# Kernel optimization log

Measured on AMD Instinct MI355X. Metric: run time of the kernel, lower is better.

The kernel has to match this reference:

```python
import jax, jax.numpy as jnp
import numpy as np

D = 2048      # hidden_size
H = 16        # num_attention_heads
KVH = 4       # num_key_value_heads
HD = 128      # head_dim
E = 32        # num_experts
TOPK = 8      # num_experts_per_tok
F = 768       # moe_intermediate_size
EPS = 1e-6
THETA = 1000000.0
B, S = 2, 1024


def setup_inputs() -> dict:
    key = jax.random.key(0)
    ks = jax.random.split(key, 16)
    sc = lambda *shape: 1.0 / np.sqrt(shape[-2] if len(shape) > 1 else shape[0])
    return {
        "hidden_states": jax.random.normal(ks[0], (B, S, D), jnp.float32),
        "attention_mask": jnp.ones((B, S), jnp.bool_),
        "input_ln_scale": jnp.ones((D,), jnp.float32),
        "post_ln_scale": jnp.ones((D,), jnp.float32),
        "q_w": jax.random.normal(ks[1], (D, H * HD), jnp.float32) * sc(D, H * HD),
        "k_w": jax.random.normal(ks[2], (D, KVH * HD), jnp.float32) * sc(D, KVH * HD),
        "v_w": jax.random.normal(ks[3], (D, KVH * HD), jnp.float32) * sc(D, KVH * HD),
        "o_w": jax.random.normal(ks[4], (H * HD, D), jnp.float32) * sc(H * HD, D),
        "q_norm_scale": jnp.ones((HD,), jnp.float32),
        "k_norm_scale": jnp.ones((HD,), jnp.float32),
        "gate_w": jax.random.normal(ks[5], (D, E), jnp.float32) * sc(D, E),
        "gate_proj": jax.random.normal(ks[6], (E, D, F), jnp.float32) * sc(E, D, F),
        "up_proj": jax.random.normal(ks[7], (E, D, F), jnp.float32) * sc(E, D, F),
        "down_proj": jax.random.normal(ks[8], (E, F, D), jnp.float32) * sc(E, F, D),
    }


def _rms(x, scale):
    return x * jax.lax.rsqrt(jnp.mean(x * x, axis=-1, keepdims=True) + EPS) * scale


def _rope(x):
    # x: [B, S, h, HD]
    half = HD // 2
    inv_freq = 1.0 / (THETA ** (jnp.arange(0, half, dtype=jnp.float32) / half))
    freqs = jnp.arange(x.shape[1], dtype=jnp.float32)[:, None] * inv_freq  # [S, HD/2]
    cos = jnp.concatenate([jnp.cos(freqs)] * 2, axis=-1)[None, :, None, :]
    sin = jnp.concatenate([jnp.sin(freqs)] * 2, axis=-1)[None, :, None, :]
    rot = jnp.concatenate([-x[..., half:], x[..., :half]], axis=-1)
    return x * cos + rot * sin


def _forward(hidden_states, attention_mask, input_ln_scale, post_ln_scale,
             q_w, k_w, v_w, o_w, q_norm_scale, k_norm_scale,
             gate_w, gate_proj, up_proj, down_proj):
    b, s, _ = hidden_states.shape
    residual = hidden_states
    h = _rms(hidden_states, input_ln_scale)

    # ---- Qwen3 attention (GQA + per-head RMSNorm + RoPE, causal) ----
    q = _rms((h @ q_w).reshape(b, s, H, HD), q_norm_scale)
    k = _rms((h @ k_w).reshape(b, s, KVH, HD), k_norm_scale)
    v = (h @ v_w).reshape(b, s, KVH, HD)
    q, k = _rope(q), _rope(k)
    rep = H // KVH
    k = jnp.repeat(k, rep, axis=2)  # [B,S,H,HD]
    v = jnp.repeat(v, rep, axis=2)
    scores = jnp.einsum('bqhd,bkhd->bhqk', q, k) * (HD ** -0.5)
    causal = jnp.tril(jnp.ones((s, s), jnp.bool_))
    mask = causal[None, None] & attention_mask[:, None, None, :]
    scores = jnp.where(mask, scores, jnp.finfo(scores.dtype).min)
    attn = jax.nn.softmax(scores, axis=-1)
    ctx = jnp.einsum('bhqk,bkhd->bqhd', attn, v).reshape(b, s, H * HD)
    h = residual + ctx @ o_w

    # ---- MoE block ----
    residual = h
    x = _rms(h, post_ln_scale).reshape(-1, D)  # [N, D]
    router_logits = x @ gate_w                 # [N, E]
    routing_weights, selected = jax.lax.top_k(router_logits, k=TOPK)
    routing_weights = jax.nn.softmax(routing_weights, axis=-1)
    sel_flat = jnp.ravel(selected)                     # [N*K]
    x_exp = jnp.repeat(x, TOPK, axis=0)                # [N*K, D]
    sort_idx = jnp.argsort(sel_flat)
    unsort_idx = jnp.argsort(sort_idx)
    x_sorted = x_exp[sort_idx]
    group_sizes = jnp.bincount(sel_flat, length=E)
    gate_out = jax.lax.ragged_dot(x_sorted, gate_proj, group_sizes)
    up_out = jax.lax.ragged_dot(x_sorted, up_proj, group_sizes)
    activated = jax.nn.silu(gate_out) * up_out
    down_out = jax.lax.ragged_dot(activated, down_proj, group_sizes)
    unsorted = down_out[unsort_idx].reshape(-1, TOPK, D)
    moe_out = (unsorted * routing_weights[..., None]).sum(axis=1).reshape(b, s, D)
    return residual + moe_out


def reference(hidden_states, attention_mask, input_ln_scale, post_ln_scale,
              q_w, k_w, v_w, o_w, q_norm_scale, k_norm_scale,
              gate_w, gate_proj, up_proj, down_proj):
    return _forward(hidden_states, attention_mask, input_ln_scale, post_ln_scale,
                    q_w, k_w, v_w, o_w, q_norm_scale, k_norm_scale,
                    gate_w, gate_proj, up_proj, down_proj)
```

## Files before the change

kernel.cpp:

```cpp
#include <hip/hip_runtime.h>
#include <hip/hip_bf16.h>

#define D_ 2048
#define H_ 16
#define KVH_ 4
#define HD_ 128
#define E_ 32
#define TOPK_ 8
#define F_ 768
#define NB_ 2
#define SS_ 1024
#define NT_ 2048
#define NPAIR_ 16384

typedef __attribute__((ext_vector_type(8))) short short8;
typedef __attribute__((ext_vector_type(4))) float floatx4;
typedef __attribute__((ext_vector_type(4))) unsigned int uintx4;
typedef __attribute__((ext_vector_type(4))) unsigned short ushortx4;

__device__ __forceinline__ unsigned short f2bf(float f) {
  union { float f; unsigned u; } v; v.f = f;
  unsigned r = v.u + 0x7FFFu + ((v.u >> 16) & 1u);
  return (unsigned short)(r >> 16);
}
__device__ __forceinline__ float bf2f(unsigned short h) {
  union { unsigned u; float f; } v; v.u = ((unsigned)h) << 16;
  return v.f;
}
__device__ __forceinline__ void split2(float v, unsigned short& hi, unsigned short& lo) {
  unsigned short h = f2bf(v);
  hi = h;
  lo = f2bf(v - bf2f(h));
}
__device__ __forceinline__ void gload16(const unsigned short* g, unsigned short* l) {
  __builtin_amdgcn_global_load_lds(
      (const __attribute__((address_space(1))) unsigned int*)g,
      (__attribute__((address_space(3))) unsigned int*)l, 16, 0, 0);
}

__global__ __launch_bounds__(256) void tconv_kernel(const float* __restrict__ src,
                                                    unsigned short* __restrict__ dst,
                                                    int R, int C) {
  size_t off = (size_t)blockIdx.z * R * C;
  src += off; dst += off;
  __shared__ float t[32][33];
  int c0 = blockIdx.x * 32, r0 = blockIdx.y * 32;
  int row = threadIdx.x >> 3, c4 = (threadIdx.x & 7) * 4;
  float4 v = *(const float4*)(src + (size_t)(r0 + row) * C + c0 + c4);
  t[row][c4 + 0] = v.x; t[row][c4 + 1] = v.y; t[row][c4 + 2] = v.z; t[row][c4 + 3] = v.w;
  __syncthreads();
  ushortx4 o = { f2bf(t[c4 + 0][row]), f2bf(t[c4 + 1][row]),
                 f2bf(t[c4 + 2][row]), f2bf(t[c4 + 3][row]) };
  *(ushortx4*)(dst + (size_t)(c0 + row) * R + r0 + c4) = o;
}

__global__ __launch_bounds__(256) void tsplit_kernel(const float* __restrict__ src,
                                                     unsigned short* __restrict__ dhi,
                                                     unsigned short* __restrict__ dlo,
                                                     int R, int C) {
  __shared__ float t[32][33];
  int c0 = blockIdx.x * 32, r0 = blockIdx.y * 32;
  int row = threadIdx.x >> 3, c4 = (threadIdx.x & 7) * 4;
  float4 v = *(const float4*)(src + (size_t)(r0 + row) * C + c0 + c4);
  t[row][c4 + 0] = v.x; t[row][c4 + 1] = v.y; t[row][c4 + 2] = v.z; t[row][c4 + 3] = v.w;
  __syncthreads();
  ushortx4 oh, ol;
  #pragma unroll
  for (int i = 0; i < 4; ++i) {
    unsigned short hi, lo;
    split2(t[c4 + i][row], hi, lo);
    oh[i] = hi; ol[i] = lo;
  }
  size_t didx = (size_t)(c0 + row) * R + r0 + c4;
  *(ushortx4*)(dhi + didx) = oh;
  *(ushortx4*)(dlo + didx) = ol;
}

template<int MODE>
__global__ __launch_bounds__(256) void rms_kernel(const float* __restrict__ in,
                                                  const float* __restrict__ sc,
                                                  float* __restrict__ outf,
                                                  unsigned short* __restrict__ o1,
                                                  unsigned short* __restrict__ o2) {
  __shared__ float red[4];
  int row = blockIdx.x, tid = threadIdx.x;
  const float4* x4 = (const float4*)(in + (size_t)row * D_);
  float4 a = x4[tid], b = x4[tid + 256];
  float ss = a.x*a.x + a.y*a.y + a.z*a.z + a.w*a.w
           + b.x*b.x + b.y*b.y + b.z*b.z + b.w*b.w;
  #pragma unroll
  for (int off = 1; off < 64; off <<= 1) ss += __shfl_xor(ss, off);
  if ((tid & 63) == 0) red[tid >> 6] = ss;
  __syncthreads();
  float r = rsqrtf((red[0] + red[1] + red[2] + red[3]) * (1.0f / D_) + 1e-6f);
  const float4* s4 = (const float4*)sc;
  float4 sa = s4[tid], sb = s4[tid + 256];
  float va[8] = { a.x*r*sa.x, a.y*r*sa.y, a.z*r*sa.z, a.w*r*sa.w,
                  b.x*r*sb.x, b.y*r*sb.y, b.z*r*sb.z, b.w*r*sb.w };
  if (MODE == 0) {
    ushortx4 h0, l0, h1, l1;
    #pragma unroll
    for (int i = 0; i < 4; ++i) { unsigned short h, l; split2(va[i], h, l); h0[i] = h; l0[i] = l; }
    #pragma unroll
    for (int i = 0; i < 4; ++i) { unsigned short h, l; split2(va[4 + i], h, l); h1[i] = h; l1[i] = l; }
    *(ushortx4*)(o1 + (size_t)row * D_ + tid * 4) = h0;
    *(ushortx4*)(o2 + (size_t)row * D_ + tid * 4) = l0;
    *(ushortx4*)(o1 + (size_t)row * D_ + 1024 + tid * 4) = h1;
    *(ushortx4*)(o2 + (size_t)row * D_ + 1024 + tid * 4) = l1;
  } else {
    *(float4*)(outf + (size_t)row * D_ + tid * 4) = make_float4(va[0], va[1], va[2], va[3]);
    *(float4*)(outf + (size_t)row * D_ + 1024 + tid * 4) = make_float4(va[4], va[5], va[6], va[7]);
    ushortx4 h0 = { f2bf(va[0]), f2bf(va[1]), f2bf(va[2]), f2bf(va[3]) };
    ushortx4 h1 = { f2bf(va[4]), f2bf(va[5]), f2bf(va[6]), f2bf(va[7]) };
    *(ushortx4*)(o1 + (size_t)row * D_ + tid * 4) = h0;
    *(ushortx4*)(o1 + (size_t)row * D_ + 1024 + tid * 4) = h1;
  }
}

template<int EPI>
__global__ __launch_bounds__(256) void gemm_bb(const unsigned short* __restrict__ Ahi,
                                               const unsigned short* __restrict__ Alo,
                                               const unsigned short* __restrict__ Bhi,
                                               const unsigned short* __restrict__ Blo,
                                               const float* __restrict__ res,
                                               float* __restrict__ out,
                                               int M, int Nn, int K) {
  __shared__ unsigned short Ah[64 * 72], Al[64 * 72], Bh[64 * 72], Bl[64 * 72];
  int tid = threadIdx.x, l = tid & 63, wid = tid >> 6;
  int lr = l & 15, lk = (l >> 4) * 8;
  int m0 = blockIdx.y * 64, n0 = blockIdx.x * 64;
  int wr = (wid >> 1) * 32, wc = (wid & 1) * 32;
  int srow = tid >> 3, sch = (tid & 7) * 8;
  size_t aoff[2], boff[2];
  int loff[2];
  #pragma unroll
  for (int i = 0; i < 2; ++i) {
    aoff[i] = (size_t)(m0 + i * 32 + srow) * K + sch;
    boff[i] = (size_t)(n0 + i * 32 + srow) * K + sch;
    loff[i] = (i * 32 + srow) * 72 + sch;
  }
  floatx4 acc[2][2];
  #pragma unroll
  for (int i = 0; i < 2; ++i)
    #pragma unroll
    for (int j = 0; j < 2; ++j) acc[i][j] = (floatx4){0.f, 0.f, 0.f, 0.f};
  for (int k0 = 0; k0 < K; k0 += 64) {
    uintx4 vah[2], val[2], vbh[2], vbl[2];
    #pragma unroll
    for (int i = 0; i < 2; ++i) {
      vah[i] = *(const uintx4*)(Ahi + aoff[i] + k0);
      val[i] = *(const uintx4*)(Alo + aoff[i] + k0);
      vbh[i] = *(const uintx4*)(Bhi + boff[i] + k0);
      vbl[i] = *(const uintx4*)(Blo + boff[i] + k0);
    }
    __syncthreads();
    #pragma unroll
    for (int i = 0; i < 2; ++i) {
      *(uintx4*)&Ah[loff[i]] = vah[i];
      *(uintx4*)&Al[loff[i]] = val[i];
      *(uintx4*)&Bh[loff[i]] = vbh[i];
      *(uintx4*)&Bl[loff[i]] = vbl[i];
    }
    __syncthreads();
    #pragma unroll
    for (int ks = 0; ks < 2; ++ks) {
      short8 ah[2], al_[2], bh[2], bl_[2];
      #pragma unroll
      for (int i = 0; i < 2; ++i) {
        ah[i]  = *(const short8*)&Ah[(wr + i * 16 + lr) * 72 + ks * 32 + lk];
        al_[i] = *(const short8*)&Al[(wr + i * 16 + lr) * 72 + ks * 32 + lk];
        bh[i]  = *(const short8*)&Bh[(wc + i * 16 + lr) * 72 + ks * 32 + lk];
        bl_[i] = *(const short8*)&Bl[(wc + i * 16 + lr) * 72 + ks * 32 + lk];
      }
      #pragma unroll
      for (int i = 0; i < 2; ++i)
        #pragma unroll
        for (int j = 0; j < 2; ++j) {
          acc[i][j] = __builtin_amdgcn_mfma_f32_16x16x32_bf16(ah[i], bh[j], acc[i][j], 0, 0, 0);
          acc[i][j] = __builtin_amdgcn_mfma_f32_16x16x32_bf16(ah[i], bl_[j], acc[i][j], 0, 0, 0);
          acc[i][j] = __builtin_amdgcn_mfma_f32_16x16x32_bf16(al_[i], bh[j], acc[i][j], 0, 0, 0);
        }
    }
  }
  int rq = (l >> 4) * 4;
  #pragma unroll
  for (int i = 0; i < 2; ++i)
    #pragma unroll
    for (int j = 0; j < 2; ++j)
      #pragma unroll
      for (int r = 0; r < 4; ++r) {
        size_t idx = (size_t)(m0 + wr + i * 16 + rq + r) * Nn + (n0 + wc + j * 16 + lr);
        float v = acc[i][j][r];
        if (EPI == 1) v += res[idx];
        out[idx] = v;
      }
}

template<int EPI>
__global__ __launch_bounds__(256) void gemm_bb128g(const unsigned short* __restrict__ Ahi,
                                                   const unsigned short* __restrict__ Alo,
                                                   const unsigned short* __restrict__ Bhi,
                                                   const unsigned short* __restrict__ Blo,
                                                   const float* __restrict__ res,
                                                   float* __restrict__ out,
                                                   int M, int Nn, int K) {
  int g = blockIdx.x;
  int nwg = gridDim.x;
  int per = nwg >> 3;
  int sw = (g & 7) * per + (g >> 3);
  int my = M >> 7;
  int xt = sw / my, yt = sw - xt * my;
  int m0 = yt * 128, n0 = xt * 128;
  __shared__ unsigned short Ah[2][128 * 32], Al[2][128 * 32];
  __shared__ unsigned short Bh[2][128 * 32], Bl[2][128 * 32];
  int tid = threadIdx.x, l = tid & 63, wid = tid >> 6;
  int lr = l & 15, lk = (l >> 4) * 8;
  int wr = (wid >> 1) * 64, wc = (wid & 1) * 64;
  int srl = l >> 2;
  int sch = ((l & 3) ^ (srl & 3)) * 8;
  size_t aoffs[2], boffs[2];
  int ldo[2];
  #pragma unroll
  for (int i = 0; i < 2; ++i) {
    int r = wid * 32 + i * 16 + srl;
    aoffs[i] = (size_t)(m0 + r) * K + sch;
    boffs[i] = (size_t)(n0 + r) * K + sch;
    ldo[i] = (wid * 32 + i * 16) * 32;
  }
  floatx4 acc[4][4];
  #pragma unroll
  for (int i = 0; i < 4; ++i)
    #pragma unroll
    for (int j = 0; j < 4; ++j) acc[i][j] = (floatx4){0.f, 0.f, 0.f, 0.f};

  auto stage = [&](int sel, int k0) {
    #pragma unroll
    for (int i = 0; i < 2; ++i) {
      gload16(Ahi + aoffs[i] + k0, &Ah[sel][ldo[i]]);
      gload16(Alo + aoffs[i] + k0, &Al[sel][ldo[i]]);
      gload16(Bhi + boffs[i] + k0, &Bh[sel][ldo[i]]);
      gload16(Blo + boffs[i] + k0, &Bl[sel][ldo[i]]);
    }
  };

  int rsw = ((l >> 4) ^ (lr & 3)) << 3;
  stage(0, 0);
  asm volatile("s_waitcnt vmcnt(0)" ::: "memory");
  __syncthreads();
  for (int k0 = 0; k0 < K; k0 += 32) {
    int cur = (k0 >> 5) & 1;
    if (k0 + 32 < K) stage(cur ^ 1, k0 + 32);
    short8 ah[4], al_[4];
    #pragma unroll
    for (int i = 0; i < 4; ++i) {
      int ao = (wr + i * 16 + lr) * 32 + rsw;
      ah[i]  = *(const short8*)&Ah[cur][ao];
      al_[i] = *(const short8*)&Al[cur][ao];
    }
    #pragma unroll
    for (int j = 0; j < 4; ++j) {
      int bo = (wc + j * 16 + lr) * 32 + rsw;
      short8 bh  = *(const short8*)&Bh[cur][bo];
      short8 bl_ = *(const short8*)&Bl[cur][bo];
      #pragma unroll
      for (int i = 0; i < 4; ++i) {
        acc[i][j] = __builtin_amdgcn_mfma_f32_16x16x32_bf16(ah[i], bh, acc[i][j], 0, 0, 0);
        acc[i][j] = __builtin_amdgcn_mfma_f32_16x16x32_bf16(ah[i], bl_, acc[i][j], 0, 0, 0);
        acc[i][j] = __builtin_amdgcn_mfma_f32_16x16x32_bf16(al_[i], bh, acc[i][j], 0, 0, 0);
      }
    }
    asm volatile("s_waitcnt vmcnt(0)" ::: "memory");
    __syncthreads();
  }
  int rq = (l >> 4) * 4;
  #pragma unroll
  for (int i = 0; i < 4; ++i)
    #pragma unroll
    for (int j = 0; j < 4; ++j)
      #pragma unroll
      for (int r = 0; r < 4; ++r) {
        size_t idx = (size_t)(m0 + wr + i * 16 + rq + r) * Nn + (n0 + wc + j * 16 + lr);
        float v = acc[i][j][r];
        if (EPI == 1) v += res[idx];
        out[idx] = v;
      }
}

__global__ __launch_bounds__(256) void qknorm_rope_kernel(const float* __restrict__ qb,
                                                          const float* __restrict__ kb,
                                                          const float* __restrict__ qs,
                                                          const float* __restrict__ ks,
                                                          unsigned short* __restrict__ qhi,
                                                          unsigned short* __restrict__ qlo,
                                                          unsigned short* __restrict__ khi,
                                                          unsigned short* __restrict__ klo) {
  int gw = blockIdx.x * 4 + (threadIdx.x >> 6);
  int l = threadIdx.x & 63;
  const float* ptr; const float* sc; unsigned short *dhi, *dlo; int t;
  size_t orow;
  if (gw < NT_ * H_) { ptr = qb + (size_t)gw * HD_; sc = qs; dhi = qhi; dlo = qlo; orow = (size_t)gw * HD_; t = gw >> 4; }
  else { int r = gw - NT_ * H_; ptr = kb + (size_t)r * HD_; sc = ks; dhi = khi; dlo = klo; orow = (size_t)r * HD_; t = r >> 2; }
  int pos = t & (SS_ - 1);
  float2 x = *(const float2*)(ptr + 2 * l);
  float p2 = x.x * x.x + x.y * x.y;
  #pragma unroll
  for (int off = 1; off < 64; off <<= 1) p2 += __shfl_xor(p2, off);
  float rms = rsqrtf(p2 * (1.0f / HD_) + 1e-6f);
  float nx = x.x * rms * sc[2 * l];
  float ny = x.y * rms * sc[2 * l + 1];
  int j0 = (2 * l) & 63;
  float ang0 = pos * __expf(-(float)j0 * (13.815510557964274f / 64.0f));
  float ang1 = pos * __expf(-(float)(j0 + 1) * (13.815510557964274f / 64.0f));
  float s0, c0, s1, c1;
  sincosf(ang0, &s0, &c0);
  sincosf(ang1, &s1, &c1);
  float ox = __shfl_xor(nx, 32);
  float oy = __shfl_xor(ny, 32);
  float r0, r1;
  if (l < 32) { r0 = nx * c0 - ox * s0; r1 = ny * c1 - oy * s1; }
  else        { r0 = nx * c0 + ox * s0; r1 = ny * c1 + oy * s1; }
  unsigned short h0, l0, h1, l1;
  split2(r0, h0, l0);
  split2(r1, h1, l1);
  *(unsigned*)(dhi + orow + 2 * l) = (unsigned)h0 | ((unsigned)h1 << 16);
  *(unsigned*)(dlo + orow + 2 * l) = (unsigned)l0 | ((unsigned)l1 << 16);
}

__global__ __launch_bounds__(256) void vsplit_kernel(const float* __restrict__ vbuf,
                                                     unsigned short* __restrict__ vthi,
                                                     unsigned short* __restrict__ vtlo) {
  int d0 = blockIdx.x * 32, s0 = blockIdx.y * 32, bk = blockIdx.z;
  int b = bk >> 2, kvh = bk & 3;
  __shared__ float t[32][33];
  int row = threadIdx.x >> 3, c4 = (threadIdx.x & 7) * 4;
  float4 v = *(const float4*)(vbuf + ((size_t)(b * SS_ + s0 + row) * KVH_ + kvh) * HD_ + d0 + c4);
  t[row][c4 + 0] = v.x; t[row][c4 + 1] = v.y; t[row][c4 + 2] = v.z; t[row][c4 + 3] = v.w;
  __syncthreads();
  ushortx4 oh, ol;
  #pragma unroll
  for (int i = 0; i < 4; ++i) {
    unsigned short hi, lo;
    split2(t[c4 + i][row], hi, lo);
    oh[i] = hi; ol[i] = lo;
  }
  size_t idx = ((size_t)(b * KVH_ + kvh) * HD_ + d0 + row) * SS_ + s0 + c4;
  *(ushortx4*)(vthi + idx) = oh;
  *(ushortx4*)(vtlo + idx) = ol;
}

__global__ __launch_bounds__(256) void attn_kernel(const unsigned short* __restrict__ qhi,
                                                   const unsigned short* __restrict__ qlo,
                                                   const unsigned short* __restrict__ khi,
                                                   const unsigned short* __restrict__ klo,
                                                   const unsigned short* __restrict__ vthi,
                                                   const unsigned short* __restrict__ vtlo,
                                                   unsigned short* __restrict__ ctx_hi,
                                                   unsigned short* __restrict__ ctx_lo) {
  int qt = blockIdx.x, h = blockIdx.y, b = blockIdx.z;
  int kvh = h >> 2;
  int tid = threadIdx.x, l = tid & 63, wid = tid >> 6;
  int lr = l & 15, lk = (l >> 4) * 8;
  __shared__ unsigned short Kh[2][32 * 128], Kl[2][32 * 128];
  __shared__ unsigned short Vh[2][128 * 32], Vl[2][128 * 32];
  __shared__ unsigned short Ph[64 * 40], Pl[64 * 40];
  int qt0 = qt * 64;

  size_t qrow = ((size_t)((b * SS_ + qt0 + wid * 16 + lr) * H_) + h) * HD_;
  short8 qfh[4], qfl[4];
  #pragma unroll
  for (int t = 0; t < 4; ++t) {
    qfh[t] = *(const short8*)(qhi + qrow + t * 32 + lk);
    qfl[t] = *(const short8*)(qlo + qrow + t * 32 + lk);
  }

  float m[4], sum[4];
  #pragma unroll
  for (int r = 0; r < 4; ++r) { m[r] = -__builtin_inff(); sum[r] = 0.f; }
  floatx4 o[8];
  #pragma unroll
  for (int cb = 0; cb < 8; ++cb) o[cb] = (floatx4){0.f, 0.f, 0.f, 0.f};

  size_t vbase = ((size_t)(b * KVH_ + kvh) * HD_) * SS_;
  int nt = 2 * qt + 2;

  auto stage = [&](int sel, int kt) {
    int k0 = kt * 32;
    #pragma unroll
    for (int i = 0; i < 2; ++i) {
      int r = wid * 8 + i * 4 + (l >> 4);
      int ch = (l & 15) ^ (r & 7);
      size_t gk = ((size_t)((b * SS_ + k0 + r) * KVH_) + kvh) * HD_ + ch * 8;
      gload16(khi + gk, &Kh[sel][(wid * 8 + i * 4) * 128]);
      gload16(klo + gk, &Kl[sel][(wid * 8 + i * 4) * 128]);
    }
    #pragma unroll
    for (int i = 0; i < 2; ++i) {
      int r = wid * 32 + i * 16 + (l >> 2);
      int ch = (l & 3) ^ (r & 3);
      size_t gv = vbase + (size_t)r * SS_ + k0 + ch * 8;
      gload16(vthi + gv, &Vh[sel][(wid * 32 + i * 16) * 32]);
      gload16(vtlo + gv, &Vl[sel][(wid * 32 + i * 16) * 32]);
    }
  };

  stage(0, 0);
  asm volatile("s_waitcnt vmcnt(0)" ::: "memory");
  __syncthreads();

  for (int kt = 0; kt < nt; ++kt) {
    int cur = kt & 1;
    if (kt + 1 < nt) stage(cur ^ 1, kt + 1);
    int k0 = kt * 32;
    float sv[2][4];
    #pragma unroll
    for (int kbk = 0; kbk < 2; ++kbk) {
      int kr = kbk * 16 + lr;
      floatx4 s = (floatx4){0.f, 0.f, 0.f, 0.f};
      #pragma unroll
      for (int t = 0; t < 4; ++t) {
        int co = kr * 128 + (((t * 4 + (l >> 4)) ^ (lr & 7)) << 3);
        short8 kfh = *(const short8*)&Kh[cur][co];
        short8 kfl = *(const short8*)&Kl[cur][co];
        s = __builtin_amdgcn_mfma_f32_16x16x32_bf16(qfh[t], kfh, s, 0, 0, 0);
        s = __builtin_amdgcn_mfma_f32_16x16x32_bf16(qfh[t], kfl, s, 0, 0, 0);
        s = __builtin_amdgcn_mfma_f32_16x16x32_bf16(qfl[t], kfh, s, 0, 0, 0);
      }
      int key = k0 + kr;
      #pragma unroll
      for (int r = 0; r < 4; ++r) {
        int q = qt0 + wid * 16 + (l >> 4) * 4 + r;
        float x = s[r] * 0.08838834764831845f;
        sv[kbk][r] = (key <= q) ? x : -1e30f;
      }
    }
    float f[4], p[2][4];
    #pragma unroll
    for (int r = 0; r < 4; ++r) {
      float tm = fmaxf(sv[0][r], sv[1][r]);
      tm = fmaxf(tm, __shfl_xor(tm, 1));
      tm = fmaxf(tm, __shfl_xor(tm, 2));
      tm = fmaxf(tm, __shfl_xor(tm, 4));
      tm = fmaxf(tm, __shfl_xor(tm, 8));
      float mn = fmaxf(m[r], tm);
      f[r] = __expf(m[r] - mn);
      m[r] = mn;
      float rs = 0.f;
      #pragma unroll
      for (int kbk = 0; kbk < 2; ++kbk) { p[kbk][r] = __expf(sv[kbk][r] - mn); rs += p[kbk][r]; }
      rs += __shfl_xor(rs, 1); rs += __shfl_xor(rs, 2);
      rs += __shfl_xor(rs, 4); rs += __shfl_xor(rs, 8);
      sum[r] = sum[r] * f[r] + rs;
    }
    #pragma unroll
    for (int kbk = 0; kbk < 2; ++kbk)
      #pragma unroll
      for (int r = 0; r < 4; ++r)
        split2(p[kbk][r],
               Ph[(wid * 16 + (l >> 4) * 4 + r) * 40 + kbk * 16 + lr],
               Pl[(wid * 16 + (l >> 4) * 4 + r) * 40 + kbk * 16 + lr]);
    #pragma unroll
    for (int cb = 0; cb < 8; ++cb)
      #pragma unroll
      for (int r = 0; r < 4; ++r) o[cb][r] = o[cb][r] * f[r];
    int pco = (wid * 16 + lr) * 40 + lk;
    short8 pah = *(const short8*)&Ph[pco];
    short8 pal = *(const short8*)&Pl[pco];
    #pragma unroll
    for (int cb = 0; cb < 8; ++cb) {
      int vo = (cb * 16 + lr) * 32 + (((l >> 4) ^ (lr & 3)) << 3);
      short8 vbh = *(const short8*)&Vh[cur][vo];
      short8 vbl = *(const short8*)&Vl[cur][vo];
      o[cb] = __builtin_amdgcn_mfma_f32_16x16x32_bf16(pah, vbh, o[cb], 0, 0, 0);
      o[cb] = __builtin_amdgcn_mfma_f32_16x16x32_bf16(pah, vbl, o[cb], 0, 0, 0);
      o[cb] = __builtin_amdgcn_mfma_f32_16x16x32_bf16(pal, vbh, o[cb], 0, 0, 0);
    }
    asm volatile("s_waitcnt vmcnt(0)" ::: "memory");
    __syncthreads();
  }
  #pragma unroll
  for (int cb = 0; cb < 8; ++cb)
    #pragma unroll
    for (int r = 0; r < 4; ++r) {
      int q = qt0 + wid * 16 + (l >> 4) * 4 + r;
      int d = cb * 16 + lr;
      float val = o[cb][r] / sum[r];
      unsigned short hi, lo;
      split2(val, hi, lo);
      size_t idx = ((size_t)(b * SS_ + q)) * (H_ * HD_) + h * HD_ + d;
      ctx_hi[idx] = hi;
      ctx_lo[idx] = lo;
    }
}

__global__ __launch_bounds__(256) void router_kernel(const float* __restrict__ x2,
                                                     const float* __restrict__ gw,
                                                     float* __restrict__ logits) {
  int t = blockIdx.x * 4 + (threadIdx.x >> 6);
  int l = threadIdx.x & 63;
  float acc[32];
  #pragma unroll
  for (int e = 0; e < 32; ++e) acc[e] = 0.f;
  for (int i = 0; i < 32; ++i) {
    int d = i * 64 + l;
    float xv = x2[(size_t)t * D_ + d];
    const float4* wr = (const float4*)(gw + (size_t)d * E_);
    #pragma unroll
    for (int j = 0; j < 8; ++j) {
      float4 wv = wr[j];
      acc[4 * j + 0] += xv * wv.x; acc[4 * j + 1] += xv * wv.y;
      acc[4 * j + 2] += xv * wv.z; acc[4 * j + 3] += xv * wv.w;
    }
  }
  #pragma unroll
  for (int e = 0; e < 32; ++e) {
    acc[e] += __shfl_xor(acc[e], 1);  acc[e] += __shfl_xor(acc[e], 2);
    acc[e] += __shfl_xor(acc[e], 4);  acc[e] += __shfl_xor(acc[e], 8);
    acc[e] += __shfl_xor(acc[e], 16); acc[e] += __shfl_xor(acc[e], 32);
  }
  if (l == 0) {
    #pragma unroll
    for (int e = 0; e < 32; ++e) logits[(size_t)t * E_ + e] = acc[e];
  }
}

__global__ void topk_kernel(const float* __restrict__ logits, int* __restrict__ sel,
                            float* __restrict__ wts, int* __restrict__ counts) {
  int t = blockIdx.x * blockDim.x + threadIdx.x;
  if (t >= NT_) return;
  float v[32];
  for (int e = 0; e < 32; ++e) v[e] = logits[(size_t)t * E_ + e];
  float val[8]; int idx[8];
  for (int k = 0; k < 8; ++k) {
    float best = -__builtin_inff(); int bi = 0;
    for (int e = 0; e < 32; ++e) if (v[e] > best) { best = v[e]; bi = e; }
    val[k] = best; idx[k] = bi; v[bi] = -__builtin_inff();
  }
  float mx = val[0], s = 0.f; float ex[8];
  for (int k = 0; k < 8; ++k) { ex[k] = expf(val[k] - mx); s += ex[k]; }
  float inv = 1.f / s;
  for (int k = 0; k < 8; ++k) {
    sel[t * 8 + k] = idx[k];
    wts[t * 8 + k] = ex[k] * inv;
    atomicAdd(&counts[idx[k]], 1);
  }
}

__global__ void scan_kernel(const int* __restrict__ counts, int* __restrict__ offs,
                            int* __restrict__ cursors) {
  if (threadIdx.x == 0) {
    int c = 0;
    for (int e = 0; e < E_; ++e) { offs[e] = c; cursors[e] = c; c += counts[e]; }
  }
}

__global__ void scatter_kernel(const int* __restrict__ sel, const float* __restrict__ wts,
                               int* __restrict__ cursors, int* __restrict__ pair_t,
                               float* __restrict__ pair_w) {
  int g = blockIdx.x * blockDim.x + threadIdx.x;
  if (g >= NPAIR_) return;
  int e = sel[g];
  int p = atomicAdd(&cursors[e], 1);
  pair_t[p] = g >> 3;
  pair_w[p] = wts[g];
}

__global__ __launch_bounds__(256, 2) void gateup_kernel(const unsigned short* __restrict__ xbf,
                                                        const unsigned short* __restrict__ gT,
                                                        const unsigned short* __restrict__ uT,
                                                        const int* __restrict__ counts,
                                                        const int* __restrict__ offs,
                                                        const int* __restrict__ pair_t,
                                                        const float* __restrict__ pair_w,
                                                        unsigned short* __restrict__ act) {
  int g = blockIdx.x;
  int rr = g & 127;
  int lg = (g & ~127) | (((rr & 7) << 4) | (rr >> 3));
  int e = lg / 192;
  int rem = lg - e * 192;
  int xt = rem >> 4, yt = rem & 15;
  int cnt = counts[e];
  int r0 = yt * 128;
  if (r0 >= cnt) return;
  int base = offs[e];
  int n0 = xt * 64;
  const unsigned short* G = gT + (size_t)e * F_ * D_;
  const unsigned short* U = uT + (size_t)e * F_ * D_;
  __shared__ unsigned short As[2][128 * 64], Gs[2][64 * 64], Us[2][64 * 64];
  int tid = threadIdx.x, l = tid & 63, wid = tid >> 6;
  int lr = l & 15, lk = (l >> 4) * 8;
  int lrow = l >> 3;
  int csw = ((l & 7) ^ lrow) * 8;
  const unsigned short* asrc[4];
  #pragma unroll
  for (int t = 0; t < 4; ++t) {
    int rowt = wid * 32 + t * 8 + lrow;
    int cr = r0 + rowt; if (cr > cnt - 1) cr = cnt - 1;
    asrc[t] = xbf + (size_t)pair_t[base + cr] * D_ + csw;
  }
  const unsigned short *gsrc[2], *usrc[2];
  #pragma unroll
  for (int t = 0; t < 2; ++t) {
    int rowt = wid * 16 + t * 8 + lrow;
    gsrc[t] = G + (size_t)(n0 + rowt) * D_ + csw;
    usrc[t] = U + (size_t)(n0 + rowt) * D_ + csw;
  }
  floatx4 ag[2][4], au[2][4];
  #pragma unroll
  for (int i = 0; i < 2; ++i)
    #pragma unroll
    for (int j = 0; j < 4; ++j) { ag[i][j] = (floatx4){0.f,0.f,0.f,0.f}; au[i][j] = (floatx4){0.f,0.f,0.f,0.f}; }
  int swz = (lr & 7) << 3;

  auto stage = [&](int sel, int kofs) {
    #pragma unroll
    for (int t = 0; t < 4; ++t)
      gload16(asrc[t] + kofs, &As[sel][(wid * 32 + t * 8) * 64]);
    #pragma unroll
    for (int t = 0; t < 2; ++t) {
      gload16(gsrc[t] + kofs, &Gs[sel][(wid * 16 + t * 8) * 64]);
      gload16(usrc[t] + kofs, &Us[sel][(wid * 16 + t * 8) * 64]);
    }
  };

  stage(0, 0);
  asm volatile("s_waitcnt vmcnt(0)" ::: "memory");
  __syncthreads();
  for (int k0 = 0; k0 < D_; k0 += 64) {
    int cur = (k0 >> 6) & 1;
    if (k0 + 64 < D_) stage(cur ^ 1, k0 + 64);
    #pragma unroll
    for (int ks = 0; ks < 2; ++ks) {
      int co = (ks * 32 + lk) ^ swz;
      short8 a[2], gg[4], uu[4];
      #pragma unroll
      for (int i = 0; i < 2; ++i)
        a[i] = *(const short8*)&As[cur][(wid * 32 + i * 16 + lr) * 64 + co];
      #pragma unroll
      for (int j = 0; j < 4; ++j) {
        gg[j] = *(const short8*)&Gs[cur][(j * 16 + lr) * 64 + co];
        uu[j] = *(const short8*)&Us[cur][(j * 16 + lr) * 64 + co];
      }
      #pragma unroll
      for (int i = 0; i < 2; ++i)
        #pragma unroll
        for (int j = 0; j < 4; ++j) {
          ag[i][j] = __builtin_amdgcn_mfma_f32_16x16x32_bf16(a[i], gg[j], ag[i][j], 0, 0, 0);
          au[i][j] = __builtin_amdgcn_mfma_f32_16x16x32_bf16(a[i], uu[j], au[i][j], 0, 0, 0);
        }
    }
    asm volatile("s_waitcnt vmcnt(0)" ::: "memory");
    __syncthreads();
  }
  int rq = (l >> 4) * 4;
  #pragma unroll
  for (int i = 0; i < 2; ++i)
    #pragma unroll
    for (int r = 0; r < 4; ++r) {
      int rowl = wid * 32 + i * 16 + rq + r;
      if (r0 + rowl < cnt) {
        int p = base + r0 + rowl;
        float pw = pair_w[p];
        size_t orow = (size_t)p * F_;
        #pragma unroll
        for (int j = 0; j < 4; ++j) {
          float gv = ag[i][j][r], uv = au[i][j][r];
          float a = (gv / (1.f + __expf(-gv))) * uv * pw;
          act[orow + n0 + j * 16 + lr] = f2bf(a);
        }
      }
    }
}

__global__ __launch_bounds__(256, 2) void down_kernel(const unsigned short* __restrict__ act,
                                                      const unsigned short* __restrict__ dT,
                                                      const int* __restrict__ counts,
                                                      const int* __restrict__ offs,
                                                      const int* __restrict__ pair_t,
                                                      float* __restrict__ out) {
  int g = blockIdx.x;
  int rr = g & 127;
  int lg = (g & ~127) | (((rr & 7) << 4) | (rr >> 3));
  int e = lg >> 8;
  int rem = lg & 255;
  int xt = rem >> 4, yt = rem & 15;
  int cnt = counts[e];
  int r0 = yt * 128;
  if (r0 >= cnt) return;
  int base = offs[e];
  int n0 = xt * 128;
  const unsigned short* B = dT + (size_t)e * ((size_t)D_ * F_);
  __shared__ unsigned short As[2][128 * 64], Bs[2][128 * 64];
  int tid = threadIdx.x, l = tid & 63, wid = tid >> 6;
  int lr = l & 15, lk = (l >> 4) * 8;
  int wr = (wid >> 1) * 64, wc = (wid & 1) * 64;
  int lrow = l >> 3;
  int csw = ((l & 7) ^ lrow) * 8;
  const unsigned short *asrc[4], *bsrc[4];
  #pragma unroll
  for (int t = 0; t < 4; ++t) {
    int rowt = wid * 32 + t * 8 + lrow;
    int cr = r0 + rowt; if (cr > cnt - 1) cr = cnt - 1;
    asrc[t] = act + (size_t)(base + cr) * F_ + csw;
    bsrc[t] = B + (size_t)(n0 + rowt) * F_ + csw;
  }
  floatx4 acc[4][4];
  #pragma unroll
  for (int i = 0; i < 4; ++i)
    #pragma unroll
    for (int j = 0; j < 4; ++j) acc[i][j] = (floatx4){0.f, 0.f, 0.f, 0.f};
  int swz = (lr & 7) << 3;

  auto stage = [&](int sel, int kofs) {
    #pragma unroll
    for (int t = 0; t < 4; ++t) {
      gload16(asrc[t] + kofs, &As[sel][(wid * 32 + t * 8) * 64]);
      gload16(bsrc[t] + kofs, &Bs[sel][(wid * 32 + t * 8) * 64]);
    }
  };

  stage(0, 0);
  asm volatile("s_waitcnt vmcnt(0)" ::: "memory");
  __syncthreads();
  for (int k0 = 0; k0 < F_; k0 += 64) {
    int cur = (k0 >> 6) & 1;
    if (k0 + 64 < F_) stage(cur ^ 1, k0 + 64);
    #pragma unroll
    for (int ks = 0; ks < 2; ++ks) {
      int co = (ks * 32 + lk) ^ swz;
      short8 a[4], b_[4];
      #pragma unroll
      for (int i = 0; i < 4; ++i) {
        a[i]  = *(const short8*)&As[cur][(wr + i * 16 + lr) * 64 + co];
        b_[i] = *(const short8*)&Bs[cur][(wc + i * 16 + lr) * 64 + co];
      }
      #pragma unroll
      for (int i = 0; i < 4; ++i)
        #pragma unroll
        for (int j = 0; j < 4; ++j)
          acc[i][j] = __builtin_amdgcn_mfma_f32_16x16x32_bf16(a[i], b_[j], acc[i][j], 0, 0, 0);
    }
    asm volatile("s_waitcnt vmcnt(0)" ::: "memory");
    __syncthreads();
  }
  int rq = (l >> 4) * 4;
  #pragma unroll
  for (int i = 0; i < 4; ++i)
    #pragma unroll
    for (int r = 0; r < 4; ++r) {
      int rowl = wr + i * 16 + rq + r;
      if (r0 + rowl < cnt) {
        int p = base + r0 + rowl;
        int tk = pair_t[p];
        #pragma unroll
        for (int j = 0; j < 4; ++j)
          atomicAdd(out + (size_t)tk * D_ + n0 + wc + j * 16 + lr, acc[i][j][r]);
      }
    }
}

extern "C" void kernel_launch(void* const* d_in, const int* in_sizes, int n_in,
                              void* d_out, int out_size, void* d_ws, size_t ws_size,
                              hipStream_t stream) {
  const float* hidden  = (const float*)d_in[0];
  const float* in_ln   = (const float*)d_in[2];
  const float* post_ln = (const float*)d_in[3];
  const float* q_w     = (const float*)d_in[4];
  const float* k_w     = (const float*)d_in[5];
  const float* v_w     = (const float*)d_in[6];
  const float* o_w     = (const float*)d_in[7];
  const float* q_ns    = (const float*)d_in[8];
  const float* k_ns    = (const float*)d_in[9];
  const float* gate_w  = (const float*)d_in[10];
  const float* gate_p  = (const float*)d_in[11];
  const float* up_p    = (const float*)d_in[12];
  const float* down_p  = (const float*)d_in[13];
  float* out = (float*)d_out;

  char* w = (char*)d_ws;
  size_t off = 0;
  auto alloc = [&](size_t b) { char* p = w + off; off += (b + 255) & ~(size_t)255; return p; };
  unsigned short* qThi = (unsigned short*)alloc((size_t)2048 * 2048 * 2);
  unsigned short* qTlo = (unsigned short*)alloc((size_t)2048 * 2048 * 2);
  unsigned short* kThi = (unsigned short*)alloc((size_t)512 * 2048 * 2);
  unsigned short* kTlo = (unsigned short*)alloc((size_t)512 * 2048 * 2);
  unsigned short* vThi = (unsigned short*)alloc((size_t)512 * 2048 * 2);
  unsigned short* vTlo = (unsigned short*)alloc((size_t)512 * 2048 * 2);
  unsigned short* oThi = (unsigned short*)alloc((size_t)2048 * 2048 * 2);
  unsigned short* oTlo = (unsigned short*)alloc((size_t)2048 * 2048 * 2);
  unsigned short* gT   = (unsigned short*)alloc((size_t)E_ * F_ * D_ * 2);
  unsigned short* uT   = (unsigned short*)alloc((size_t)E_ * F_ * D_ * 2);
  unsigned short* dT   = (unsigned short*)alloc((size_t)E_ * D_ * F_ * 2);
  unsigned short* h_hi = (unsigned short*)alloc((size_t)NT_ * D_ * 2);
  unsigned short* h_lo = (unsigned short*)alloc((size_t)NT_ * D_ * 2);
  float* qbuf  = (float*)alloc((size_t)NT_ * H_ * HD_ * 4);
  float* kbuf  = (float*)alloc((size_t)NT_ * KVH_ * HD_ * 4);
  float* vbuf  = (float*)alloc((size_t)NT_ * KVH_ * HD_ * 4);
  unsigned short* qhi = (unsigned short*)alloc((size_t)NT_ * H_ * HD_ * 2);
  unsigned short* qlo = (unsigned short*)alloc((size_t)NT_ * H_ * HD_ * 2);
  unsigned short* khi = (unsigned short*)alloc((size_t)NT_ * KVH_ * HD_ * 2);
  unsigned short* klo = (unsigned short*)alloc((size_t)NT_ * KVH_ * HD_ * 2);
  unsigned short* vthi = (unsigned short*)alloc((size_t)NT_ * KVH_ * HD_ * 2);
  unsigned short* vtlo = (unsigned short*)alloc((size_t)NT_ * KVH_ * HD_ * 2);
  unsigned short* ctx_hi = (unsigned short*)alloc((size_t)NT_ * H_ * HD_ * 2);
  unsigned short* ctx_lo = (unsigned short*)alloc((size_t)NT_ * H_ * HD_ * 2);
  float* x2    = (float*)alloc((size_t)NT_ * D_ * 4);
  unsigned short* x2bf = (unsigned short*)alloc((size_t)NT_ * D_ * 2);
  float* logits = (float*)alloc((size_t)NT_ * E_ * 4);
  int*   sel    = (int*)alloc((size_t)NT_ * TOPK_ * 4);
  float* wts    = (float*)alloc((size_t)NT_ * TOPK_ * 4);
  int*   counts = (int*)alloc(E_ * 4);
  int*   offs   = (int*)alloc(E_ * 4);
  int*   curs   = (int*)alloc(E_ * 4);
  int*   pair_t = (int*)alloc((size_t)NPAIR_ * 4);
  float* pair_w = (float*)alloc((size_t)NPAIR_ * 4);
  unsigned short* act = (unsigned short*)alloc((size_t)NPAIR_ * F_ * 2);

  tsplit_kernel<<<dim3(64, 64), 256, 0, stream>>>(q_w, qThi, qTlo, 2048, 2048);
  tsplit_kernel<<<dim3(16, 64), 256, 0, stream>>>(k_w, kThi, kTlo, 2048, 512);
  tsplit_kernel<<<dim3(16, 64), 256, 0, stream>>>(v_w, vThi, vTlo, 2048, 512);
  tsplit_kernel<<<dim3(64, 64), 256, 0, stream>>>(o_w, oThi, oTlo, 2048, 2048);
  tconv_kernel<<<dim3(24, 64, 32), 256, 0, stream>>>(gate_p, gT, 2048, 768);
  tconv_kernel<<<dim3(24, 64, 32), 256, 0, stream>>>(up_p, uT, 2048, 768);
  tconv_kernel<<<dim3(64, 24, 32), 256, 0, stream>>>(down_p, dT, 768, 2048);

  rms_kernel<0><<<NT_, 256, 0, stream>>>(hidden, in_ln, nullptr, h_hi, h_lo);
  gemm_bb128g<0><<<256, 256, 0, stream>>>(h_hi, h_lo, qThi, qTlo, nullptr, qbuf, NT_, 2048, 2048);
  gemm_bb<0><<<dim3(8, 32), 256, 0, stream>>>(h_hi, h_lo, kThi, kTlo, nullptr, kbuf, NT_, 512, 2048);
  gemm_bb<0><<<dim3(8, 32), 256, 0, stream>>>(h_hi, h_lo, vThi, vTlo, nullptr, vbuf, NT_, 512, 2048);
  qknorm_rope_kernel<<<(NT_ * (H_ + KVH_)) / 4, 256, 0, stream>>>(qbuf, kbuf, q_ns, k_ns,
                                                                  qhi, qlo, khi, klo);
  vsplit_kernel<<<dim3(HD_ / 32, SS_ / 32, NB_ * KVH_), 256, 0, stream>>>(vbuf, vthi, vtlo);
  attn_kernel<<<dim3(SS_ / 64, H_, NB_), 256, 0, stream>>>(qhi, qlo, khi, klo, vthi, vtlo,
                                                           ctx_hi, ctx_lo);
  gemm_bb128g<1><<<256, 256, 0, stream>>>(ctx_hi, ctx_lo, oThi, oTlo, hidden, out, NT_, 2048, 2048);
  rms_kernel<1><<<NT_, 256, 0, stream>>>(out, post_ln, x2, x2bf, nullptr);
  (void)hipMemsetAsync(counts, 0, E_ * 4, stream);
  router_kernel<<<NT_ / 4, 256, 0, stream>>>(x2, gate_w, logits);
  topk_kernel<<<NT_ / 256, 256, 0, stream>>>(logits, sel, wts, counts);
  scan_kernel<<<1, 64, 0, stream>>>(counts, offs, curs);
  scatter_kernel<<<NPAIR_ / 256, 256, 0, stream>>>(sel, wts, curs, pair_t, pair_w);
  gateup_kernel<<<12 * 16 * 32, 256, 0, stream>>>(x2bf, gT, uT, counts, offs, pair_t, pair_w, act);
  down_kernel<<<16 * 16 * 32, 256, 0, stream>>>(act, dT, counts, offs, pair_t, out);
}
```

Before: 1.134 ms.

## Enlarge MoE GEMM tiles to 256 rows with 512-thread blocks

Both expert GEMM kernels move to 512-thread blocks with 256-row tiles. The gate/up tile grows to 256x128 and the down tile to 256x128, and the wave-to-subtile mapping and block-swizzle remapping change to match. This raises reuse of the weight tiles staged in LDS and cuts the number of blocks that reload the same expert weights. In exchange it uses more LDS per block, allows only one block per CU, and wastes more work on partially filled tiles for experts with uneven token counts.

```diff
diff --git a/kernel.cpp b/kernel.cpp
--- a/kernel.cpp
+++ b/kernel.cpp
@@ -564,7 +564,7 @@
   pair_w[p] = wts[g];
 }
 
-__global__ __launch_bounds__(256, 2) void gateup_kernel(const unsigned short* __restrict__ xbf,
+__global__ __launch_bounds__(512, 1) void gateup_kernel(const unsigned short* __restrict__ xbf,
                                                         const unsigned short* __restrict__ gT,
                                                         const unsigned short* __restrict__ uT,
                                                         const int* __restrict__ counts,
@@ -573,19 +573,19 @@
                                                         const float* __restrict__ pair_w,
                                                         unsigned short* __restrict__ act) {
   int g = blockIdx.x;
-  int rr = g & 127;
-  int lg = (g & ~127) | (((rr & 7) << 4) | (rr >> 3));
-  int e = lg / 192;
-  int rem = lg - e * 192;
-  int xt = rem >> 4, yt = rem & 15;
+  int rr = g & 63;
+  int lg = (g & ~63) | (((rr & 7) << 3) | (rr >> 3));
+  int e = lg / 48;
+  int rem = lg - e * 48;
+  int xt = rem >> 3, yt = rem & 7;
   int cnt = counts[e];
-  int r0 = yt * 128;
+  int r0 = yt * 256;
   if (r0 >= cnt) return;
   int base = offs[e];
-  int n0 = xt * 64;
+  int n0 = xt * 128;
   const unsigned short* G = gT + (size_t)e * F_ * D_;
   const unsigned short* U = uT + (size_t)e * F_ * D_;
-  __shared__ unsigned short As[2][128 * 64], Gs[2][64 * 64], Us[2][64 * 64];
+  __shared__ unsigned short As[2][256 * 64], Gs[2][128 * 64], Us[2][128 * 64];
   int tid = threadIdx.x, l = tid & 63, wid = tid >> 6;
   int lr = l & 15, lk = (l >> 4) * 8;
   int lrow = l >> 3;
@@ -604,11 +604,13 @@
     gsrc[t] = G + (size_t)(n0 + rowt) * D_ + csw;
     usrc[t] = U + (size_t)(n0 + rowt) * D_ + csw;
   }
-  floatx4 ag[2][4], au[2][4];
-  #pragma unroll
-  for (int i = 0; i < 2; ++i)
-    #pragma unroll
-    for (int j = 0; j < 4; ++j) { ag[i][j] = (floatx4){0.f,0.f,0.f,0.f}; au[i][j] = (floatx4){0.f,0.f,0.f,0.f}; }
+  int wm = wid >> 2;
+  int wn = wid & 3;
+  floatx4 ag[8][2], au[8][2];
+  #pragma unroll
+  for (int i = 0; i < 8; ++i)
+    #pragma unroll
+    for (int j = 0; j < 2; ++j) { ag[i][j] = (floatx4){0.f,0.f,0.f,0.f}; au[i][j] = (floatx4){0.f,0.f,0.f,0.f}; }
   int swz = (lr & 7) << 3;
 
   auto stage = [&](int sel, int kofs) {
@@ -631,78 +633,83 @@
     #pragma unroll
     for (int ks = 0; ks < 2; ++ks) {
       int co = (ks * 32 + lk) ^ swz;
-      short8 a[2], gg[4], uu[4];
-      #pragma unroll
-      for (int i = 0; i < 2; ++i)
-        a[i] = *(const short8*)&As[cur][(wid * 32 + i * 16 + lr) * 64 + co];
-      #pragma unroll
-      for (int j = 0; j < 4; ++j) {
-        gg[j] = *(const short8*)&Gs[cur][(j * 16 + lr) * 64 + co];
-        uu[j] = *(const short8*)&Us[cur][(j * 16 + lr) * 64 + co];
-      }
-      #pragma unroll
-      for (int i = 0; i < 2; ++i)
+      short8 gg[2], uu[2];
+      #pragma unroll
+      for (int j = 0; j < 2; ++j) {
+        gg[j] = *(const short8*)&Gs[cur][(wn * 32 + j * 16 + lr) * 64 + co];
+        uu[j] = *(const short8*)&Us[cur][(wn * 32 + j * 16 + lr) * 64 + co];
+      }
+      #pragma unroll
+      for (int i = 0; i < 8; ++i) {
+        short8 a = *(const short8*)&As[cur][(wm * 128 + i * 16 + lr) * 64 + co];
         #pragma unroll
-        for (int j = 0; j < 4; ++j) {
-          ag[i][j] = __builtin_amdgcn_mfma_f32_16x16x32_bf16(a[i], gg[j], ag[i][j], 0, 0, 0);
-          au[i][j] = __builtin_amdgcn_mfma_f32_16x16x32_bf16(a[i], uu[j], au[i][j], 0, 0, 0);
+        for (int j = 0; j < 2; ++j) {
+          ag[i][j] = __builtin_amdgcn_mfma_f32_16x16x32_bf16(a, gg[j], ag[i][j], 0, 0, 0);
+          au[i][j] = __builtin_amdgcn_mfma_f32_16x16x32_bf16(a, uu[j], au[i][j], 0, 0, 0);
         }
+      }
     }
     asm volatile("s_waitcnt vmcnt(0)" ::: "memory");
     __syncthreads();
   }
   int rq = (l >> 4) * 4;
   #pragma unroll
-  for (int i = 0; i < 2; ++i)
+  for (int i = 0; i < 8; ++i)
     #pragma unroll
     for (int r = 0; r < 4; ++r) {
-      int rowl = wid * 32 + i * 16 + rq + r;
+      int rowl = wm * 128 + i * 16 + rq + r;
       if (r0 + rowl < cnt) {
         int p = base + r0 + rowl;
         float pw = pair_w[p];
         size_t orow = (size_t)p * F_;
         #pragma unroll
-        for (int j = 0; j < 4; ++j) {
+        for (int j = 0; j < 2; ++j) {
           float gv = ag[i][j][r], uv = au[i][j][r];
           float a = (gv / (1.f + __expf(-gv))) * uv * pw;
-          act[orow + n0 + j * 16 + lr] = f2bf(a);
+          act[orow + n0 + wn * 32 + j * 16 + lr] = f2bf(a);
         }
       }
     }
 }
 
-__global__ __launch_bounds__(256, 2) void down_kernel(const unsigned short* __restrict__ act,
+__global__ __launch_bounds__(512, 1) void down_kernel(const unsigned short* __restrict__ act,
                                                       const unsigned short* __restrict__ dT,
                                                       const int* __restrict__ counts,
                                                       const int* __restrict__ offs,
                                                       const int* __restrict__ pair_t,
                                                       float* __restrict__ out) {
   int g = blockIdx.x;
-  int rr = g & 127;
-  int lg = (g & ~127) | (((rr & 7) << 4) | (rr >> 3));
-  int e = lg >> 8;
-  int rem = lg & 255;
-  int xt = rem >> 4, yt = rem & 15;
+  int rr = g & 63;
+  int lg = (g & ~63) | (((rr & 7) << 3) | (rr >> 3));
+  int e = lg >> 7;
+  int rem = lg & 127;
+  int xt = rem >> 3, yt = rem & 7;
   int cnt = counts[e];
-  int r0 = yt * 128;
+  int r0 = yt * 256;
   if (r0 >= cnt) return;
   int base = offs[e];
   int n0 = xt * 128;
   const unsigned short* B = dT + (size_t)e * ((size_t)D_ * F_);
-  __shared__ unsigned short As[2][128 * 64], Bs[2][128 * 64];
+  __shared__ unsigned short As[2][256 * 64], Bs[2][128 * 64];
   int tid = threadIdx.x, l = tid & 63, wid = tid >> 6;
   int lr = l & 15, lk = (l >> 4) * 8;
-  int wr = (wid >> 1) * 64, wc = (wid & 1) * 64;
   int lrow = l >> 3;
   int csw = ((l & 7) ^ lrow) * 8;
-  const unsigned short *asrc[4], *bsrc[4];
+  const unsigned short* asrc[4];
   #pragma unroll
   for (int t = 0; t < 4; ++t) {
     int rowt = wid * 32 + t * 8 + lrow;
     int cr = r0 + rowt; if (cr > cnt - 1) cr = cnt - 1;
     asrc[t] = act + (size_t)(base + cr) * F_ + csw;
+  }
+  const unsigned short* bsrc[2];
+  #pragma unroll
+  for (int t = 0; t < 2; ++t) {
+    int rowt = wid * 16 + t * 8 + lrow;
     bsrc[t] = B + (size_t)(n0 + rowt) * F_ + csw;
   }
+  int wm = wid >> 1;
+  int wn = wid & 1;
   floatx4 acc[4][4];
   #pragma unroll
   for (int i = 0; i < 4; ++i)
@@ -712,10 +719,11 @@
 
   auto stage = [&](int sel, int kofs) {
     #pragma unroll
-    for (int t = 0; t < 4; ++t) {
+    for (int t = 0; t < 4; ++t)
       gload16(asrc[t] + kofs, &As[sel][(wid * 32 + t * 8) * 64]);
-      gload16(bsrc[t] + kofs, &Bs[sel][(wid * 32 + t * 8) * 64]);
-    }
+    #pragma unroll
+    for (int t = 0; t < 2; ++t)
+      gload16(bsrc[t] + kofs, &Bs[sel][(wid * 16 + t * 8) * 64]);
   };
 
   stage(0, 0);
@@ -729,10 +737,11 @@
       int co = (ks * 32 + lk) ^ swz;
       short8 a[4], b_[4];
       #pragma unroll
-      for (int i = 0; i < 4; ++i) {
-        a[i]  = *(const short8*)&As[cur][(wr + i * 16 + lr) * 64 + co];
-        b_[i] = *(const short8*)&Bs[cur][(wc + i * 16 + lr) * 64 + co];
-      }
+      for (int i = 0; i < 4; ++i)
+        a[i] = *(const short8*)&As[cur][(wm * 64 + i * 16 + lr) * 64 + co];
+      #pragma unroll
+      for (int j = 0; j < 4; ++j)
+        b_[j] = *(const short8*)&Bs[cur][(wn * 64 + j * 16 + lr) * 64 + co];
       #pragma unroll
       for (int i = 0; i < 4; ++i)
         #pragma unroll
@@ -747,13 +756,13 @@
   for (int i = 0; i < 4; ++i)
     #pragma unroll
     for (int r = 0; r < 4; ++r) {
-      int rowl = wr + i * 16 + rq + r;
+      int rowl = wm * 64 + i * 16 + rq + r;
       if (r0 + rowl < cnt) {
         int p = base + r0 + rowl;
         int tk = pair_t[p];
         #pragma unroll
         for (int j = 0; j < 4; ++j)
-          atomicAdd(out + (size_t)tk * D_ + n0 + wc + j * 16 + lr, acc[i][j][r]);
+          atomicAdd(out + (size_t)tk * D_ + n0 + wn * 64 + j * 16 + lr, acc[i][j][r]);
       }
     }
 }
@@ -839,6 +848,6 @@
   topk_kernel<<<NT_ / 256, 256, 0, stream>>>(logits, sel, wts, counts);
   scan_kernel<<<1, 64, 0, stream>>>(counts, offs, curs);
   scatter_kernel<<<NPAIR_ / 256, 256, 0, stream>>>(sel, wts, curs, pair_t, pair_w);
-  gateup_kernel<<<12 * 16 * 32, 256, 0, stream>>>(x2bf, gT, uT, counts, offs, pair_t, pair_w, act);
-  down_kernel<<<16 * 16 * 32, 256, 0, stream>>>(act, dT, counts, offs, pair_t, out);
-}
+  gateup_kernel<<<6 * 8 * 32, 512, 0, stream>>>(x2bf, gT, uT, counts, offs, pair_t, pair_w, act);
+  down_kernel<<<16 * 8 * 32, 512, 0, stream>>>(act, dT, counts, offs, pair_t, out);
+}
```

Result: slower. 1.207 ms (+6.4%).
